# Kernel tuning notes

Hardware: AMD Instinct MI355X
Metric: run time of the kernel (lower is better)

## Reference

```python
import jax, jax.numpy as jnp
import numpy as np

ARITY = 4
IN_DIM = 512
OUT_DIM = 32
BATCH = 4096


def setup_inputs() -> dict:
    key = jax.random.key(0)
    k1, k2 = jax.random.split(key)
    X = jax.random.normal(k1, (BATCH, IN_DIM, ARITY), dtype=jnp.float32)
    params = jax.random.normal(k2, (IN_DIM, 2 ** ARITY, OUT_DIM), dtype=jnp.float32)
    return {"X": X, "params": params}


def reference(X, params):
    # Multilinear simplex interpolation per (batch, channel):
    # sort the arity inputs, form barycentric-style coefficients from the sorted
    # gaps, and gather the arity param rows selected by reverse-cumsum bitmasks.
    ind_sort = jnp.argsort(X, axis=2)                       # [B, G, K] ascending order
    A_sort = jnp.take_along_axis(X, ind_sort, axis=2)       # sorted values
    coef = jnp.concatenate(
        [A_sort[:, :, :1], A_sort[:, :, 1:] - A_sort[:, :, :-1]], axis=2
    )                                                        # [B, G, K]
    bits = jnp.left_shift(1, ind_sort)                       # 2**A_ind
    # reverse cumulative sum along the sorted axis -> bitmask indices into params
    idx = jnp.flip(jnp.cumsum(jnp.flip(bits, axis=2), axis=2), axis=2)  # [B, G, K]
    g = jnp.arange(params.shape[0])[None, :, None]           # channel index [1, G, 1]
    gathered = params[g, idx]                                # [B, G, K, O]
    return jnp.einsum('bgk,bgko->bgo', coef, gathered)       # [B, G, O]
```

## Files before the change

kernel.cpp:

```cpp
#include <hip/hip_runtime.h>

#define BATCH   4096
#define IN_DIM  512
#define OUT_DIM 32
#define CH      16
#define NB      64
#define NITER   32

typedef float f32x4 __attribute__((ext_vector_type(4)));

__global__ __launch_bounds__(256) void simplex_interp_lds(
    const float* __restrict__ X,
    const float* __restrict__ params,
    float* __restrict__ out)
{
    __shared__ float lds_p[CH * 16 * OUT_DIM];
    __shared__ float lds_x[NB * CH * 4];

    const int tid = threadIdx.x;
    const int cg  = blockIdx.x & 31;
    const int bg  = blockIdx.x >> 5;
    const int b0  = bg * NB;
    const int g0  = cg * CH;

    {
        const float* src = params + (size_t)cg * (CH * 16 * OUT_DIM);
        #pragma unroll
        for (int k = 0; k < 8; ++k) {
            const int off = (k * 256 + tid) * 4;
            *reinterpret_cast<f32x4*>(&lds_p[off]) =
                *reinterpret_cast<const f32x4*>(src + off);
        }
    }
    {
        #pragma unroll
        for (int k = 0; k < 4; ++k) {
            const int chunk = k * 256 + tid;
            const int b     = chunk >> 4;
            const int pos   = chunk & 15;
            const size_t goff = ((size_t)(b0 + b) * IN_DIM + g0) * 4 + pos * 4;
            *reinterpret_cast<f32x4*>(&lds_x[b * (CH * 4) + pos * 4]) =
                __builtin_nontemporal_load(reinterpret_cast<const f32x4*>(X + goff));
        }
    }
    __syncthreads();

    const int half = tid >> 7;
    const int c    = (tid >> 3) & 15;
    const int sub  = tid & 7;
    const int g    = g0 + c;

    const float* ldsc = &lds_p[c * (16 * OUT_DIM) + sub * 4];
    const f32x4  p15  = *reinterpret_cast<const f32x4*>(ldsc + 15 * OUT_DIM);

    #pragma unroll 4
    for (int i = 0; i < NITER; ++i) {
        const int lb = 2 * i + half;
        const f32x4 xv = *reinterpret_cast<const f32x4*>(&lds_x[lb * (CH * 4) + c * 4]);

        float v0 = xv.x, v1 = xv.y, v2 = xv.z, v3 = xv.w;
        int   i0 = 0,    i1 = 1,    i2 = 2,    i3 = 3;
#define CSWAP(va, vb, ia, ib)                                            \
        {                                                                \
            bool lt = (vb) < (va);                                       \
            float tv = (va); (va) = lt ? (vb) : (va); (vb) = lt ? tv : (vb); \
            int   ti = (ia); (ia) = lt ? (ib) : (ia); (ib) = lt ? ti : (ib); \
        }
        CSWAP(v0, v1, i0, i1)
        CSWAP(v2, v3, i2, i3)
        CSWAP(v0, v2, i0, i2)
        CSWAP(v1, v3, i1, i3)
        CSWAP(v1, v2, i1, i2)
#undef CSWAP

        const float c0 = v0;
        const float c1 = v1 - v0;
        const float c2 = v2 - v1;
        const float c3 = v3 - v2;

        const int idx3 = (1 << i3);
        const int idx2 = idx3 + (1 << i2);
        const int idx1 = idx2 + (1 << i1);

        const f32x4 q1 = *reinterpret_cast<const f32x4*>(ldsc + idx1 * OUT_DIM);
        const f32x4 q2 = *reinterpret_cast<const f32x4*>(ldsc + idx2 * OUT_DIM);
        const f32x4 q3 = *reinterpret_cast<const f32x4*>(ldsc + idx3 * OUT_DIM);

        const f32x4 acc = c0 * p15 + c1 * q1 + c2 * q2 + c3 * q3;

        __builtin_nontemporal_store(acc,
            reinterpret_cast<f32x4*>(out + ((size_t)(b0 + lb) * IN_DIM + g) * OUT_DIM + sub * 4));
    }
}

extern "C" void kernel_launch(void* const* d_in, const int* in_sizes, int n_in,
                              void* d_out, int out_size, void* d_ws, size_t ws_size,
                              hipStream_t stream) {
    const float* X      = (const float*)d_in[0];
    const float* params = (const float*)d_in[1];
    float*       out    = (float*)d_out;

    const int nblocks = (IN_DIM / CH) * (BATCH / NB);
    simplex_interp_lds<<<nblocks, 256, 0, stream>>>(X, params, out);
}
```

Before: 65.66 us.

## Process multiple batch groups per block with register-prefetched X loads

Halves channels per block and has each block loop over four 64-row batch groups. The next group's X tile is prefetched into registers while the current group is computed, then written to LDS between barriers. The params tile is loaded once and amortised over more batch rows, and the block count drops. Output stores switch from nontemporal to regular stores. The cost is extra barriers per group, fewer blocks to hide latency, and a different grid mapping (64 channel groups by 16 batch groups).

```diff
diff --git a/kernel.cpp b/kernel.cpp
--- a/kernel.cpp
+++ b/kernel.cpp
@@ -3,13 +3,15 @@
 #define BATCH   4096
 #define IN_DIM  512
 #define OUT_DIM 32
-#define CH      16
+#define CH      8
 #define NB      64
-#define NITER   32
+#define NGROUP  4
+#define CGRID   (IN_DIM / CH)
+#define BGRID   (BATCH / (NB * NGROUP))
 
 typedef float f32x4 __attribute__((ext_vector_type(4)));
 
-__global__ __launch_bounds__(256) void simplex_interp_lds(
+__global__ __launch_bounds__(256) void simplex_interp_persist(
     const float* __restrict__ X,
     const float* __restrict__ params,
     float* __restrict__ out)
@@ -18,78 +20,99 @@
     __shared__ float lds_x[NB * CH * 4];
 
     const int tid = threadIdx.x;
-    const int cg  = blockIdx.x & 31;
-    const int bg  = blockIdx.x >> 5;
-    const int b0  = bg * NB;
+    const int cg  = blockIdx.x & (CGRID - 1);
+    const int bg  = blockIdx.x >> 6;
     const int g0  = cg * CH;
+    const int b0  = bg * (NB * NGROUP);
 
     {
-        const float* src = params + (size_t)cg * (CH * 16 * OUT_DIM);
+        const float* src = params + (size_t)g0 * (16 * OUT_DIM);
         #pragma unroll
-        for (int k = 0; k < 8; ++k) {
+        for (int k = 0; k < 4; ++k) {
             const int off = (k * 256 + tid) * 4;
             *reinterpret_cast<f32x4*>(&lds_p[off]) =
                 *reinterpret_cast<const f32x4*>(src + off);
         }
     }
-    {
-        #pragma unroll
-        for (int k = 0; k < 4; ++k) {
-            const int chunk = k * 256 + tid;
-            const int b     = chunk >> 4;
-            const int pos   = chunk & 15;
-            const size_t goff = ((size_t)(b0 + b) * IN_DIM + g0) * 4 + pos * 4;
-            *reinterpret_cast<f32x4*>(&lds_x[b * (CH * 4) + pos * 4]) =
-                __builtin_nontemporal_load(reinterpret_cast<const f32x4*>(X + goff));
-        }
-    }
+
+    const int xchunk0 = tid;
+    const int xlb0    = xchunk0 >> 3;
+    const int xpos0   = xchunk0 & 7;
+    const int xchunk1 = 256 + tid;
+    const int xlb1    = xchunk1 >> 3;
+    const int xpos1   = xchunk1 & 7;
+
+    f32x4 ra, rb;
+    auto load_x = [&](int grp) {
+        const size_t base = ((size_t)(b0 + grp * NB) * IN_DIM + g0) * 4;
+        ra = __builtin_nontemporal_load(
+            reinterpret_cast<const f32x4*>(X + base + (size_t)xlb0 * (IN_DIM * 4) + xpos0 * 4));
+        rb = __builtin_nontemporal_load(
+            reinterpret_cast<const f32x4*>(X + base + (size_t)xlb1 * (IN_DIM * 4) + xpos1 * 4));
+    };
+    auto write_x = [&]() {
+        *reinterpret_cast<f32x4*>(&lds_x[xlb0 * (CH * 4) + xpos0 * 4]) = ra;
+        *reinterpret_cast<f32x4*>(&lds_x[xlb1 * (CH * 4) + xpos1 * 4]) = rb;
+    };
+
+    load_x(0);
+    write_x();
     __syncthreads();
 
-    const int half = tid >> 7;
-    const int c    = (tid >> 3) & 15;
-    const int sub  = tid & 7;
-    const int g    = g0 + c;
+    const int bq  = tid >> 6;
+    const int c   = (tid >> 3) & 7;
+    const int sub = tid & 7;
+    const int g   = g0 + c;
 
     const float* ldsc = &lds_p[c * (16 * OUT_DIM) + sub * 4];
     const f32x4  p15  = *reinterpret_cast<const f32x4*>(ldsc + 15 * OUT_DIM);
 
-    #pragma unroll 4
-    for (int i = 0; i < NITER; ++i) {
-        const int lb = 2 * i + half;
-        const f32x4 xv = *reinterpret_cast<const f32x4*>(&lds_x[lb * (CH * 4) + c * 4]);
+    for (int grp = 0; grp < NGROUP; ++grp) {
+        if (grp + 1 < NGROUP) load_x(grp + 1);
 
-        float v0 = xv.x, v1 = xv.y, v2 = xv.z, v3 = xv.w;
-        int   i0 = 0,    i1 = 1,    i2 = 2,    i3 = 3;
+        const int bbase = b0 + grp * NB;
+        #pragma unroll 4
+        for (int i = 0; i < NB / 4; ++i) {
+            const int lb = i * 4 + bq;
+            const f32x4 xv = *reinterpret_cast<const f32x4*>(&lds_x[lb * (CH * 4) + c * 4]);
+
+            float v0 = xv.x, v1 = xv.y, v2 = xv.z, v3 = xv.w;
+            int   i0 = 0,    i1 = 1,    i2 = 2,    i3 = 3;
 #define CSWAP(va, vb, ia, ib)                                            \
-        {                                                                \
-            bool lt = (vb) < (va);                                       \
-            float tv = (va); (va) = lt ? (vb) : (va); (vb) = lt ? tv : (vb); \
-            int   ti = (ia); (ia) = lt ? (ib) : (ia); (ib) = lt ? ti : (ib); \
-        }
-        CSWAP(v0, v1, i0, i1)
-        CSWAP(v2, v3, i2, i3)
-        CSWAP(v0, v2, i0, i2)
-        CSWAP(v1, v3, i1, i3)
-        CSWAP(v1, v2, i1, i2)
+            {                                                            \
+                bool lt = (vb) < (va);                                   \
+                float tv = (va); (va) = lt ? (vb) : (va); (vb) = lt ? tv : (vb); \
+                int   ti = (ia); (ia) = lt ? (ib) : (ia); (ib) = lt ? ti : (ib); \
+            }
+            CSWAP(v0, v1, i0, i1)
+            CSWAP(v2, v3, i2, i3)
+            CSWAP(v0, v2, i0, i2)
+            CSWAP(v1, v3, i1, i3)
+            CSWAP(v1, v2, i1, i2)
 #undef CSWAP
 
-        const float c0 = v0;
-        const float c1 = v1 - v0;
-        const float c2 = v2 - v1;
-        const float c3 = v3 - v2;
+            const float c0 = v0;
+            const float c1 = v1 - v0;
+            const float c2 = v2 - v1;
+            const float c3 = v3 - v2;
 
-        const int idx3 = (1 << i3);
-        const int idx2 = idx3 + (1 << i2);
-        const int idx1 = idx2 + (1 << i1);
+            const int idx3 = (1 << i3);
+            const int idx2 = idx3 + (1 << i2);
+            const int idx1 = idx2 + (1 << i1);
 
-        const f32x4 q1 = *reinterpret_cast<const f32x4*>(ldsc + idx1 * OUT_DIM);
-        const f32x4 q2 = *reinterpret_cast<const f32x4*>(ldsc + idx2 * OUT_DIM);
-        const f32x4 q3 = *reinterpret_cast<const f32x4*>(ldsc + idx3 * OUT_DIM);
+            const f32x4 q1 = *reinterpret_cast<const f32x4*>(ldsc + idx1 * OUT_DIM);
+            const f32x4 q2 = *reinterpret_cast<const f32x4*>(ldsc + idx2 * OUT_DIM);
+            const f32x4 q3 = *reinterpret_cast<const f32x4*>(ldsc + idx3 * OUT_DIM);
 
-        const f32x4 acc = c0 * p15 + c1 * q1 + c2 * q2 + c3 * q3;
+            const f32x4 acc = c0 * p15 + c1 * q1 + c2 * q2 + c3 * q3;
 
-        __builtin_nontemporal_store(acc,
-            reinterpret_cast<f32x4*>(out + ((size_t)(b0 + lb) * IN_DIM + g) * OUT_DIM + sub * 4));
+            *reinterpret_cast<f32x4*>(
+                out + ((size_t)(bbase + lb) * IN_DIM + g) * OUT_DIM + sub * 4) = acc;
+        }
+
+        __syncthreads();
+        if (grp + 1 < NGROUP) write_x();
+        __syncthreads();
     }
 }
 
@@ -100,6 +123,6 @@
     const float* params = (const float*)d_in[1];
     float*       out    = (float*)d_out;
 
-    const int nblocks = (IN_DIM / CH) * (BATCH / NB);
-    simplex_interp_lds<<<nblocks, 256, 0, stream>>>(X, params, out);
+    const int nblocks = CGRID * BGRID;
+    simplex_interp_persist<<<nblocks, 256, 0, stream>>>(X, params, out);
 }
```

After: 54.35 us. 1.21x faster.
